# Optimization experiments

Hardware: AMD Instinct MI355X
Metric: run time of the kernel (lower is better)

The kernel has to match this reference:

```python
import jax, jax.numpy as jnp
import numpy as np

HEAD = 8  # number of attention heads (init kwarg)


def setup_inputs() -> dict:
    key = jax.random.key(0)
    k1, k2, k3 = jax.random.split(key, 3)
    b, H, W, c = 8, 32, 32, 512
    dim = 512
    x = jax.random.normal(k1, (b, H, W, c), dtype=jnp.float32)
    # 1x1 Conv == per-pixel matmul over channels
    w_qkv = jax.random.normal(k2, (c, 3 * dim), dtype=jnp.float32) * (c ** -0.5)
    w_out = jax.random.normal(k3, (dim, dim), dtype=jnp.float32) * (dim ** -0.5)
    b_out = jnp.zeros((dim,), dtype=jnp.float32)
    return {"x": x, "w_qkv": w_qkv, "w_out": w_out, "b_out": b_out}


def reference(x, w_qkv, w_out, b_out):
    b, H, W, c = x.shape
    n = H * W
    # QKV 1x1-conv projection (no bias)
    qkv = jnp.einsum('bhwc,cd->bhwd', x, w_qkv)          # (b, H, W, 3*dim)
    qkv = qkv.reshape(b, n, HEAD, -1)                     # (b, n, head, 3*dh)
    q, k, v = jnp.split(qkv, 3, axis=-1)                  # each (b, n, head, dh)
    scale = b ** -0.5  # NOTE: source scales by batch size, reproduced faithfully
    attn = jax.nn.softmax(jnp.einsum('bihd,bjhd->bhij', q, k) * scale, axis=-1)
    out = jnp.einsum('bhij,bjhd->bihd', attn, v)          # (b, n, head, dh)
    out = out.reshape(b, H, W, -1)                        # (b, H, W, dim)
    # output 1x1-conv projection (with bias)
    return jnp.einsum('bhwc,cd->bhwd', out, w_out) + b_out
```

## Files before the change

kernel.cpp:

```cpp
#include <hip/hip_runtime.h>
#include <hip/hip_bf16.h>

typedef __bf16 bf16x8_t __attribute__((ext_vector_type(8)));
typedef float  f32x4_t  __attribute__((ext_vector_type(4)));
typedef short  s16x8_t  __attribute__((ext_vector_type(8)));

#define NTOK   1024
#define CDIM   512
#define QKVDIM 1536
#define NHEAD  8
#define DHEAD  64
#define C1EXP  0.51007088f
#define C2EXP  34.624681f

__device__ __forceinline__ float b2f(short s) {
    unsigned int u = ((unsigned int)(unsigned short)s) << 16;
    float f; __builtin_memcpy(&f, &u, 4); return f;
}
__device__ __forceinline__ short f2b(float f) {
    __bf16 h = (__bf16)f; short s; __builtin_memcpy(&s, &h, 2); return s;
}

__global__ __launch_bounds__(256) void cvt_fused(
    const float* __restrict__ x, const float* __restrict__ wq,
    short* __restrict__ xb, short* __restrict__ wqbT)
{
    int bid = blockIdx.x;
    if (bid < 2048) {
        int i = bid * 256 + threadIdx.x;
        const float* p = x + (size_t)i * 8;
        float4 a = *(const float4*)p, b = *(const float4*)(p + 4);
        s16x8_t v;
        v[0]=f2b(a.x); v[1]=f2b(a.y); v[2]=f2b(a.z); v[3]=f2b(a.w);
        v[4]=f2b(b.x); v[5]=f2b(b.y); v[6]=f2b(b.z); v[7]=f2b(b.w);
        *(s16x8_t*)(xb + (size_t)i * 8) = v;
    } else {
        int i = (bid - 2048) * 256 + threadIdx.x;
        int k = i / QKVDIM, n = i % QKVDIM;
        wqbT[(size_t)n * 512 + k] = f2b(wq[i]);
    }
}

__global__ __launch_bounds__(256) void cvtT(const float* __restrict__ in,
                                            short* __restrict__ out,
                                            int K, int N)
{
    int i = blockIdx.x * 256 + threadIdx.x;
    if (i < K * N) {
        int k = i / N, n = i % N;
        out[(size_t)n * K + k] = f2b(in[i]);
    }
}

template <int N, bool BIAS, bool OUTF32>
__global__ __launch_bounds__(256) void gemm128(
    const short* __restrict__ A, const short* __restrict__ Bt,
    const float* __restrict__ bias, void* __restrict__ C)
{
    __shared__ __align__(16) short Al[128 * 64];
    __shared__ __align__(16) short Bl[128 * 64];

    const int t = threadIdx.x;
    const int N0 = blockIdx.x * 128, M0 = blockIdx.y * 128;
    const int w = t >> 6, lane = t & 63;
    const int quad = lane >> 4, mr = lane & 15;
    const int wm = (w >> 1) * 64, wn = (w & 1) * 64;

    int srow[4], soff[4];
#pragma unroll
    for (int r = 0; r < 4; ++r) {
        int ci = r * 256 + t;
        srow[r] = ci >> 3;
        soff[r] = (ci & 7) * 8;
    }
    const short* Ag = A  + (size_t)M0 * 512;
    const short* Bg = Bt + (size_t)N0 * 512;

    s16x8_t ar[4], br[4];
#pragma unroll
    for (int r = 0; r < 4; ++r) {
        ar[r] = *(const s16x8_t*)(Ag + (size_t)srow[r] * 512 + soff[r]);
        br[r] = *(const s16x8_t*)(Bg + (size_t)srow[r] * 512 + soff[r]);
    }

    f32x4_t acc[4][4];
#pragma unroll
    for (int ms = 0; ms < 4; ++ms)
#pragma unroll
        for (int ns = 0; ns < 4; ++ns) acc[ms][ns] = f32x4_t{0.f,0.f,0.f,0.f};

#pragma unroll 1
    for (int kc = 0; kc < 8; ++kc) {
        __syncthreads();
#pragma unroll
        for (int r = 0; r < 4; ++r) {
            int lds = srow[r] * 64 + (((soff[r] >> 3) ^ (srow[r] & 7)) * 8);
            *(s16x8_t*)(Al + lds) = ar[r];
            *(s16x8_t*)(Bl + lds) = br[r];
        }
        __syncthreads();
        if (kc < 7) {
            int k0 = (kc + 1) * 64;
#pragma unroll
            for (int r = 0; r < 4; ++r) {
                ar[r] = *(const s16x8_t*)(Ag + (size_t)srow[r] * 512 + k0 + soff[r]);
                br[r] = *(const s16x8_t*)(Bg + (size_t)srow[r] * 512 + k0 + soff[r]);
            }
        }
#pragma unroll
        for (int kh = 0; kh < 2; ++kh) {
            bf16x8_t af[4], bf[4];
#pragma unroll
            for (int ms = 0; ms < 4; ++ms) {
                int rr = wm + ms * 16 + mr;
                af[ms] = *(const bf16x8_t*)(Al + rr * 64 + (((kh * 4 + quad) ^ (rr & 7)) * 8));
            }
#pragma unroll
            for (int ns = 0; ns < 4; ++ns) {
                int rr = wn + ns * 16 + mr;
                bf[ns] = *(const bf16x8_t*)(Bl + rr * 64 + (((kh * 4 + quad) ^ (rr & 7)) * 8));
            }
#pragma unroll
            for (int ms = 0; ms < 4; ++ms)
#pragma unroll
                for (int ns = 0; ns < 4; ++ns)
                    acc[ms][ns] = __builtin_amdgcn_mfma_f32_16x16x32_bf16(
                        af[ms], bf[ns], acc[ms][ns], 0, 0, 0);
        }
    }

#pragma unroll
    for (int ms = 0; ms < 4; ++ms) {
        int row = M0 + wm + ms * 16 + quad * 4;
#pragma unroll
        for (int ns = 0; ns < 4; ++ns) {
            int col = N0 + wn + ns * 16 + mr;
            float bz = BIAS ? bias[col] : 0.f;
#pragma unroll
            for (int i = 0; i < 4; ++i) {
                if constexpr (OUTF32)
                    ((float*)C)[(size_t)(row + i) * N + col] = acc[ms][ns][i] + bz;
                else
                    ((short*)C)[(size_t)(row + i) * N + col] = f2b(acc[ms][ns][i]);
            }
        }
    }
}

__global__ __launch_bounds__(256) void attn_mfma(
    const short* __restrict__ qkv, short* __restrict__ aout)
{
    __shared__ __align__(16) short Kb[2][64 * 72];
    __shared__ __align__(16) short Vb[2][64 * 72];
    __shared__ __align__(16) short Pl[4][32 * 72];

    const int t = threadIdx.x;
    const int g = blockIdx.x;
    const int qb = (g >> 3) & 7;
    const int bh = ((g >> 6) << 3) | (g & 7);
    const int h = bh & 7, b = bh >> 3;
    const int w = t >> 6, lane = t & 63;
    const int quad = lane >> 4, mr = lane & 15;

    bf16x8_t qf[2][2];
#pragma unroll
    for (int ms = 0; ms < 2; ++ms) {
        size_t qrow = (size_t)(b * NTOK + qb * 128 + w * 32 + ms * 16 + mr) * QKVDIM + h * 192;
        qf[ms][0] = *(const bf16x8_t*)(qkv + qrow + quad * 8);
        qf[ms][1] = *(const bf16x8_t*)(qkv + qrow + 32 + quad * 8);
    }

    float lsum[2][4] = {};
    f32x4_t O[2][4];
#pragma unroll
    for (int ms = 0; ms < 2; ++ms)
#pragma unroll
        for (int d = 0; d < 4; ++d) O[ms][d] = f32x4_t{0.f, 0.f, 0.f, 0.f};

    short* Pw = Pl[w];

    const int j0i = t >> 3, j1i = j0i + 32, d8 = (t & 7) * 8;
    const int pjb0 = ((j0i >> 3) ^ (t & 7)) * 8 + (j0i & 7);
    const int pjb1 = ((j1i >> 3) ^ (t & 7)) * 8 + (j1i & 7);

    s16x8_t k0r, v0r, k1r, v1r;
    {
        size_t b0 = (size_t)(b * NTOK + j0i) * QKVDIM + h * 192;
        size_t b1 = (size_t)(b * NTOK + j1i) * QKVDIM + h * 192;
        k0r = *(const s16x8_t*)(qkv + b0 + 64 + d8);
        v0r = *(const s16x8_t*)(qkv + b0 + 128 + d8);
        k1r = *(const s16x8_t*)(qkv + b1 + 64 + d8);
        v1r = *(const s16x8_t*)(qkv + b1 + 128 + d8);
    }

#pragma unroll 1
    for (int jt = 0; jt < 16; ++jt) {
        const int cur = jt & 1;
        short* Kl = Kb[cur];
        short* Vt = Vb[cur];
        *(s16x8_t*)(Kl + j0i * 72 + d8) = k0r;
        *(s16x8_t*)(Kl + j1i * 72 + d8) = k1r;
#pragma unroll
        for (int i = 0; i < 8; ++i) {
            Vt[(d8 + i) * 72 + pjb0] = v0r[i];
            Vt[(d8 + i) * 72 + pjb1] = v1r[i];
        }
        __syncthreads();

        if (jt < 15) {
            size_t b0 = (size_t)(b * NTOK + (jt + 1) * 64 + j0i) * QKVDIM + h * 192;
            size_t b1 = (size_t)(b * NTOK + (jt + 1) * 64 + j1i) * QKVDIM + h * 192;
            k0r = *(const s16x8_t*)(qkv + b0 + 64 + d8);
            v0r = *(const s16x8_t*)(qkv + b0 + 128 + d8);
            k1r = *(const s16x8_t*)(qkv + b1 + 64 + d8);
            v1r = *(const s16x8_t*)(qkv + b1 + 128 + d8);
        }

#pragma unroll
        for (int ms = 0; ms < 2; ++ms) {
            f32x4_t s[4];
#pragma unroll
            for (int js = 0; js < 4; ++js) {
                const short* kb = Kl + (js * 16 + mr) * 72 + quad * 8;
                f32x4_t a0 = __builtin_amdgcn_mfma_f32_16x16x32_bf16(
                    qf[ms][0], *(const bf16x8_t*)kb, f32x4_t{0.f,0.f,0.f,0.f}, 0, 0, 0);
                s[js] = __builtin_amdgcn_mfma_f32_16x16x32_bf16(
                    qf[ms][1], *(const bf16x8_t*)(kb + 32), a0, 0, 0, 0);
            }

            short ph[4][4];
#pragma unroll
            for (int js = 0; js < 4; ++js)
#pragma unroll
                for (int r = 0; r < 4; ++r) {
                    short hh = f2b(__builtin_amdgcn_exp2f(s[js][r] * C1EXP - C2EXP));
                    ph[js][r] = hh;
                    lsum[ms][r] += b2f(hh);
                }

            short* Pm = Pw + ms * 16 * 72;
#pragma unroll
            for (int js = 0; js < 4; ++js)
#pragma unroll
                for (int r = 0; r < 4; ++r)
                    Pm[(quad * 4 + r) * 72 +
                       (((js * 2 + (mr >> 3)) + 2 * quad) & 7) * 8 + (mr & 7)] = ph[js][r];
            bf16x8_t pa0 = *(const bf16x8_t*)(Pm + mr * 72 + ((quad     + 2 * (mr >> 2)) & 7) * 8);
            bf16x8_t pa1 = *(const bf16x8_t*)(Pm + mr * 72 + ((quad + 4 + 2 * (mr >> 2)) & 7) * 8);

#pragma unroll
            for (int d = 0; d < 4; ++d) {
                int R = d * 16 + mr;
                int rx = (R >> 3) & 7;
                const short* vb0 = Vt + R * 72 + ((quad ^ rx) * 8);
                const short* vb1 = Vt + R * 72 + (((4 + quad) ^ rx) * 8);
                O[ms][d] = __builtin_amdgcn_mfma_f32_16x16x32_bf16(
                    pa0, *(const bf16x8_t*)vb0, O[ms][d], 0, 0, 0);
                O[ms][d] = __builtin_amdgcn_mfma_f32_16x16x32_bf16(
                    pa1, *(const bf16x8_t*)vb1, O[ms][d], 0, 0, 0);
            }
        }
    }

#pragma unroll
    for (int ms = 0; ms < 2; ++ms)
#pragma unroll
        for (int r = 0; r < 4; ++r) {
            float l = lsum[ms][r];
#pragma unroll
            for (int off = 1; off < 16; off <<= 1) l += __shfl_xor(l, off);
            float inv = 1.f / l;
            size_t tok = (size_t)(b * NTOK + qb * 128 + w * 32 + ms * 16 + quad * 4 + r);
#pragma unroll
            for (int d = 0; d < 4; ++d)
                aout[tok * CDIM + h * DHEAD + d * 16 + mr] = f2b(O[ms][d][r] * inv);
        }
}

extern "C" void kernel_launch(void* const* d_in, const int* in_sizes, int n_in,
                              void* d_out, int out_size, void* d_ws, size_t ws_size,
                              hipStream_t stream)
{
    const float* x     = (const float*)d_in[0];
    const float* w_qkv = (const float*)d_in[1];
    const float* w_out = (const float*)d_in[2];
    const float* b_out = (const float*)d_in[3];
    for (int i = 0; i < n_in; ++i) {
        if      (in_sizes[i] == 4194304) x     = (const float*)d_in[i];
        else if (in_sizes[i] ==  786432) w_qkv = (const float*)d_in[i];
        else if (in_sizes[i] ==  262144) w_out = (const float*)d_in[i];
        else if (in_sizes[i] ==     512) b_out = (const float*)d_in[i];
    }

    short* qkv  = (short*)d_ws;
    short* aout = (short*)((char*)d_ws + (size_t)8192 * QKVDIM * 2);
    short* xb   = (short*)d_out;
    short* wqbT = (short*)d_out + (size_t)8192 * 512;
    short* wobT = (short*)d_ws;

    cvt_fused<<<5120, 256, 0, stream>>>(x, w_qkv, xb, wqbT);

    gemm128<QKVDIM, false, false>
        <<<dim3(QKVDIM / 128, 8192 / 128), 256, 0, stream>>>(xb, wqbT, nullptr, qkv);

    attn_mfma<<<512, 256, 0, stream>>>(qkv, aout);

    cvtT<<<1024, 256, 0, stream>>>(w_out, wobT, 512, 512);

    gemm128<CDIM, true, true>
        <<<dim3(CDIM / 128, 8192 / 128), 256, 0, stream>>>(aout, wobT, b_out, d_out);
}
```

Baseline: 152.1 us.

## Emit transposed V from QKV GEMM and simplify attention to 64-query tiles

The QKV GEMM epilogue now splits its output into a packed Q/K buffer and a per-head transposed V buffer. This lets the attention kernel load V with plain vector stores to LDS instead of scalar transposing writes. The attention kernel is restructured to 16 query rows per wave and 64 queries per block, doubling the grid to 1024 blocks. It drops LDS double buffering in favour of a second barrier and computes S transposed so P can be written with vector stores. The trade-off is more K/V reloads from global memory and strided scattered writes for V in the GEMM epilogue.

```diff
diff --git a/kernel.cpp b/kernel.cpp
--- a/kernel.cpp
+++ b/kernel.cpp
@@ -3,6 +3,7 @@
 
 typedef __bf16 bf16x8_t __attribute__((ext_vector_type(8)));
 typedef float  f32x4_t  __attribute__((ext_vector_type(4)));
+typedef short  s16x4_t  __attribute__((ext_vector_type(4)));
 typedef short  s16x8_t  __attribute__((ext_vector_type(8)));
 
 #define NTOK   1024
@@ -52,11 +53,11 @@
     }
 }
 
-template <int N, bool BIAS, bool OUTF32>
-__global__ __launch_bounds__(256) void gemm128(
+__global__ __launch_bounds__(256) void gemm_qkv(
     const short* __restrict__ A, const short* __restrict__ Bt,
-    const float* __restrict__ bias, void* __restrict__ C)
-{
+    short* __restrict__ qk, short* __restrict__ vT)
+{
+    constexpr int N = QKVDIM;
     __shared__ __align__(16) short Al[128 * 64];
     __shared__ __align__(16) short Bl[128 * 64];
 
@@ -132,6 +133,106 @@
 #pragma unroll
     for (int ms = 0; ms < 4; ++ms) {
         int row = M0 + wm + ms * 16 + quad * 4;
+        int bb = row >> 10, ti = row & 1023;
+#pragma unroll
+        for (int ns = 0; ns < 4; ++ns) {
+            int c0 = N0 + wn + ns * 16;
+            int hh = c0 / 192, r0 = c0 % 192;
+            if (r0 < 128) {
+                size_t base = (size_t)row * 1024 + hh * 128 + r0 + mr;
+#pragma unroll
+                for (int i = 0; i < 4; ++i)
+                    qk[base + (size_t)i * 1024] = f2b(acc[ms][ns][i]);
+            } else {
+                s16x4_t v4;
+#pragma unroll
+                for (int i = 0; i < 4; ++i) v4[i] = f2b(acc[ms][ns][i]);
+                *(s16x4_t*)(vT + ((size_t)(bb * 8 + hh) * 64 + (r0 - 128) + mr) * 1024 + ti) = v4;
+            }
+        }
+    }
+}
+
+template <int N, bool BIAS, bool OUTF32>
+__global__ __launch_bounds__(256) void gemm128(
+    const short* __restrict__ A, const short* __restrict__ Bt,
+    const float* __restrict__ bias, void* __restrict__ C)
+{
+    __shared__ __align__(16) short Al[128 * 64];
+    __shared__ __align__(16) short Bl[128 * 64];
+
+    const int t = threadIdx.x;
+    const int N0 = blockIdx.x * 128, M0 = blockIdx.y * 128;
+    const int w = t >> 6, lane = t & 63;
+    const int quad = lane >> 4, mr = lane & 15;
+    const int wm = (w >> 1) * 64, wn = (w & 1) * 64;
+
+    int srow[4], soff[4];
+#pragma unroll
+    for (int r = 0; r < 4; ++r) {
+        int ci = r * 256 + t;
+        srow[r] = ci >> 3;
+        soff[r] = (ci & 7) * 8;
+    }
+    const short* Ag = A  + (size_t)M0 * 512;
+    const short* Bg = Bt + (size_t)N0 * 512;
+
+    s16x8_t ar[4], br[4];
+#pragma unroll
+    for (int r = 0; r < 4; ++r) {
+        ar[r] = *(const s16x8_t*)(Ag + (size_t)srow[r] * 512 + soff[r]);
+        br[r] = *(const s16x8_t*)(Bg + (size_t)srow[r] * 512 + soff[r]);
+    }
+
+    f32x4_t acc[4][4];
+#pragma unroll
+    for (int ms = 0; ms < 4; ++ms)
+#pragma unroll
+        for (int ns = 0; ns < 4; ++ns) acc[ms][ns] = f32x4_t{0.f,0.f,0.f,0.f};
+
+#pragma unroll 1
+    for (int kc = 0; kc < 8; ++kc) {
+        __syncthreads();
+#pragma unroll
+        for (int r = 0; r < 4; ++r) {
+            int lds = srow[r] * 64 + (((soff[r] >> 3) ^ (srow[r] & 7)) * 8);
+            *(s16x8_t*)(Al + lds) = ar[r];
+            *(s16x8_t*)(Bl + lds) = br[r];
+        }
+        __syncthreads();
+        if (kc < 7) {
+            int k0 = (kc + 1) * 64;
+#pragma unroll
+            for (int r = 0; r < 4; ++r) {
+                ar[r] = *(const s16x8_t*)(Ag + (size_t)srow[r] * 512 + k0 + soff[r]);
+                br[r] = *(const s16x8_t*)(Bg + (size_t)srow[r] * 512 + k0 + soff[r]);
+            }
+        }
+#pragma unroll
+        for (int kh = 0; kh < 2; ++kh) {
+            bf16x8_t af[4], bf[4];
+#pragma unroll
+            for (int ms = 0; ms < 4; ++ms) {
+                int rr = wm + ms * 16 + mr;
+                af[ms] = *(const bf16x8_t*)(Al + rr * 64 + (((kh * 4 + quad) ^ (rr & 7)) * 8));
+            }
+#pragma unroll
+            for (int ns = 0; ns < 4; ++ns) {
+                int rr = wn + ns * 16 + mr;
+                bf[ns] = *(const bf16x8_t*)(Bl + rr * 64 + (((kh * 4 + quad) ^ (rr & 7)) * 8));
+            }
+#pragma unroll
+            for (int ms = 0; ms < 4; ++ms)
+#pragma unroll
+                for (int ns = 0; ns < 4; ++ns)
+                    acc[ms][ns] = __builtin_amdgcn_mfma_f32_16x16x32_bf16(
+                        af[ms], bf[ns], acc[ms][ns], 0, 0, 0);
+        }
+    }
+
+#pragma unroll
+    for (int ms = 0; ms < 4; ++ms) {
+        int row = M0 + wm + ms * 16 + quad * 4;
 #pragma unroll
         for (int ns = 0; ns < 4; ++ns) {
             int col = N0 + wn + ns * 16 + mr;
@@ -147,134 +248,106 @@
     }
 }
 
-__global__ __launch_bounds__(256) void attn_mfma(
-    const short* __restrict__ qkv, short* __restrict__ aout)
-{
-    __shared__ __align__(16) short Kb[2][64 * 72];
-    __shared__ __align__(16) short Vb[2][64 * 72];
-    __shared__ __align__(16) short Pl[4][32 * 72];
+__global__ __launch_bounds__(256) void attn_st(
+    const short* __restrict__ qk, const short* __restrict__ vT,
+    short* __restrict__ aout)
+{
+    __shared__ __align__(16) short Kl[64 * 72];
+    __shared__ __align__(16) short Vt[64 * 72];
+    __shared__ __align__(16) short Pl[4][16 * 72];
 
     const int t = threadIdx.x;
     const int g = blockIdx.x;
-    const int qb = (g >> 3) & 7;
-    const int bh = ((g >> 6) << 3) | (g & 7);
+    const int qt = (g >> 3) & 15;
+    const int bh = ((g >> 7) << 3) | (g & 7);
     const int h = bh & 7, b = bh >> 3;
     const int w = t >> 6, lane = t & 63;
     const int quad = lane >> 4, mr = lane & 15;
 
-    bf16x8_t qf[2][2];
-#pragma unroll
-    for (int ms = 0; ms < 2; ++ms) {
-        size_t qrow = (size_t)(b * NTOK + qb * 128 + w * 32 + ms * 16 + mr) * QKVDIM + h * 192;
-        qf[ms][0] = *(const bf16x8_t*)(qkv + qrow + quad * 8);
-        qf[ms][1] = *(const bf16x8_t*)(qkv + qrow + 32 + quad * 8);
-    }
-
-    float lsum[2][4] = {};
-    f32x4_t O[2][4];
-#pragma unroll
-    for (int ms = 0; ms < 2; ++ms)
-#pragma unroll
-        for (int d = 0; d < 4; ++d) O[ms][d] = f32x4_t{0.f, 0.f, 0.f, 0.f};
-
-    short* Pw = Pl[w];
-
-    const int j0i = t >> 3, j1i = j0i + 32, d8 = (t & 7) * 8;
-    const int pjb0 = ((j0i >> 3) ^ (t & 7)) * 8 + (j0i & 7);
-    const int pjb1 = ((j1i >> 3) ^ (t & 7)) * 8 + (j1i & 7);
-
-    s16x8_t k0r, v0r, k1r, v1r;
-    {
-        size_t b0 = (size_t)(b * NTOK + j0i) * QKVDIM + h * 192;
-        size_t b1 = (size_t)(b * NTOK + j1i) * QKVDIM + h * 192;
-        k0r = *(const s16x8_t*)(qkv + b0 + 64 + d8);
-        v0r = *(const s16x8_t*)(qkv + b0 + 128 + d8);
-        k1r = *(const s16x8_t*)(qkv + b1 + 64 + d8);
-        v1r = *(const s16x8_t*)(qkv + b1 + 128 + d8);
-    }
+    const size_t qbase = (size_t)(b * NTOK + qt * 64 + w * 16 + mr) * 1024 + h * 128;
+    const bf16x8_t qf0 = *(const bf16x8_t*)(qk + qbase + quad * 8);
+    const bf16x8_t qf1 = *(const bf16x8_t*)(qk + qbase + 32 + quad * 8);
+
+    float lsum = 0.f;
+    f32x4_t O[4];
+#pragma unroll
+    for (int d = 0; d < 4; ++d) O[d] = f32x4_t{0.f, 0.f, 0.f, 0.f};
+
+    short* Pm = Pl[w];
+
+    const int r0i = t >> 3, r1i = r0i + 32, c8 = (t & 7) * 8;
+    const size_t kgbase = (size_t)(b * NTOK) * 1024 + h * 128 + 64 + c8;
+    const size_t vgbase = (size_t)(b * 8 + h) * 64 * 1024 + c8;
+
+    s16x8_t k0r, k1r, v0r, v1r;
+    k0r = *(const s16x8_t*)(qk + kgbase + (size_t)r0i * 1024);
+    k1r = *(const s16x8_t*)(qk + kgbase + (size_t)r1i * 1024);
+    v0r = *(const s16x8_t*)(vT + vgbase + (size_t)r0i * 1024);
+    v1r = *(const s16x8_t*)(vT + vgbase + (size_t)r1i * 1024);
 
 #pragma unroll 1
     for (int jt = 0; jt < 16; ++jt) {
-        const int cur = jt & 1;
-        short* Kl = Kb[cur];
-        short* Vt = Vb[cur];
-        *(s16x8_t*)(Kl + j0i * 72 + d8) = k0r;
-        *(s16x8_t*)(Kl + j1i * 72 + d8) = k1r;
-#pragma unroll
-        for (int i = 0; i < 8; ++i) {
-            Vt[(d8 + i) * 72 + pjb0] = v0r[i];
-            Vt[(d8 + i) * 72 + pjb1] = v1r[i];
-        }
+        *(s16x8_t*)(Kl + r0i * 72 + c8) = k0r;
+        *(s16x8_t*)(Kl + r1i * 72 + c8) = k1r;
+        *(s16x8_t*)(Vt + r0i * 72 + c8) = v0r;
+        *(s16x8_t*)(Vt + r1i * 72 + c8) = v1r;
         __syncthreads();
 
         if (jt < 15) {
-            size_t b0 = (size_t)(b * NTOK + (jt + 1) * 64 + j0i) * QKVDIM + h * 192;
-            size_t b1 = (size_t)(b * NTOK + (jt + 1) * 64 + j1i) * QKVDIM + h * 192;
-            k0r = *(const s16x8_t*)(qkv + b0 + 64 + d8);
-            v0r = *(const s16x8_t*)(qkv + b0 + 128 + d8);
-            k1r = *(const s16x8_t*)(qkv + b1 + 64 + d8);
-            v1r = *(const s16x8_t*)(qkv + b1 + 128 + d8);
-        }
-
-#pragma unroll
-        for (int ms = 0; ms < 2; ++ms) {
-            f32x4_t s[4];
-#pragma unroll
-            for (int js = 0; js < 4; ++js) {
-                const short* kb = Kl + (js * 16 + mr) * 72 + quad * 8;
-                f32x4_t a0 = __builtin_amdgcn_mfma_f32_16x16x32_bf16(
-                    qf[ms][0], *(const bf16x8_t*)kb, f32x4_t{0.f,0.f,0.f,0.f}, 0, 0, 0);
-                s[js] = __builtin_amdgcn_mfma_f32_16x16x32_bf16(
-                    qf[ms][1], *(const bf16x8_t*)(kb + 32), a0, 0, 0, 0);
-            }
-
-            short ph[4][4];
-#pragma unroll
-            for (int js = 0; js < 4; ++js)
-#pragma unroll
-                for (int r = 0; r < 4; ++r) {
-                    short hh = f2b(__builtin_amdgcn_exp2f(s[js][r] * C1EXP - C2EXP));
-                    ph[js][r] = hh;
-                    lsum[ms][r] += b2f(hh);
-                }
-
-            short* Pm = Pw + ms * 16 * 72;
-#pragma unroll
-            for (int js = 0; js < 4; ++js)
-#pragma unroll
-                for (int r = 0; r < 4; ++r)
-                    Pm[(quad * 4 + r) * 72 +
-                       (((js * 2 + (mr >> 3)) + 2 * quad) & 7) * 8 + (mr & 7)] = ph[js][r];
-            bf16x8_t pa0 = *(const bf16x8_t*)(Pm + mr * 72 + ((quad     + 2 * (mr >> 2)) & 7) * 8);
-            bf16x8_t pa1 = *(const bf16x8_t*)(Pm + mr * 72 + ((quad + 4 + 2 * (mr >> 2)) & 7) * 8);
-
-#pragma unroll
-            for (int d = 0; d < 4; ++d) {
-                int R = d * 16 + mr;
-                int rx = (R >> 3) & 7;
-                const short* vb0 = Vt + R * 72 + ((quad ^ rx) * 8);
-                const short* vb1 = Vt + R * 72 + (((4 + quad) ^ rx) * 8);
-                O[ms][d] = __builtin_amdgcn_mfma_f32_16x16x32_bf16(
-                    pa0, *(const bf16x8_t*)vb0, O[ms][d], 0, 0, 0);
-                O[ms][d] = __builtin_amdgcn_mfma_f32_16x16x32_bf16(
-                    pa1, *(const bf16x8_t*)vb1, O[ms][d], 0, 0, 0);
-            }
-        }
-    }
-
-#pragma unroll
-    for (int ms = 0; ms < 2; ++ms)
-#pragma unroll
-        for (int r = 0; r < 4; ++r) {
-            float l = lsum[ms][r];
-#pragma unroll
-            for (int off = 1; off < 16; off <<= 1) l += __shfl_xor(l, off);
-            float inv = 1.f / l;
-            size_t tok = (size_t)(b * NTOK + qb * 128 + w * 32 + ms * 16 + quad * 4 + r);
-#pragma unroll
-            for (int d = 0; d < 4; ++d)
-                aout[tok * CDIM + h * DHEAD + d * 16 + mr] = f2b(O[ms][d][r] * inv);
-        }
+            int j0n = (jt + 1) * 64;
+            k0r = *(const s16x8_t*)(qk + kgbase + (size_t)(j0n + r0i) * 1024);
+            k1r = *(const s16x8_t*)(qk + kgbase + (size_t)(j0n + r1i) * 1024);
+            v0r = *(const s16x8_t*)(vT + vgbase + (size_t)r0i * 1024 + j0n);
+            v1r = *(const s16x8_t*)(vT + vgbase + (size_t)r1i * 1024 + j0n);
+        }
+
+        f32x4_t s[4];
+#pragma unroll
+        for (int jj = 0; jj < 4; ++jj) {
+            const short* kb = Kl + (jj * 16 + mr) * 72 + quad * 8;
+            f32x4_t a0 = __builtin_amdgcn_mfma_f32_16x16x32_bf16(
+                *(const bf16x8_t*)kb, qf0, f32x4_t{0.f,0.f,0.f,0.f}, 0, 0, 0);
+            s[jj] = __builtin_amdgcn_mfma_f32_16x16x32_bf16(
+                *(const bf16x8_t*)(kb + 32), qf1, a0, 0, 0, 0);
+        }
+
+#pragma unroll
+        for (int jj = 0; jj < 4; ++jj) {
+            s16x4_t pv;
+#pragma unroll
+            for (int r = 0; r < 4; ++r) {
+                short hh = f2b(__builtin_amdgcn_exp2f(s[jj][r] * C1EXP - C2EXP));
+                pv[r] = hh;
+                lsum += b2f(hh);
+            }
+            *(s16x4_t*)(Pm + mr * 72 + jj * 16 + quad * 4) = pv;
+        }
+
+        bf16x8_t pa0 = *(const bf16x8_t*)(Pm + mr * 72 + quad * 8);
+        bf16x8_t pa1 = *(const bf16x8_t*)(Pm + mr * 72 + 32 + quad * 8);
+
+#pragma unroll
+        for (int dt = 0; dt < 4; ++dt) {
+            const short* vb = Vt + (dt * 16 + mr) * 72 + quad * 8;
+            O[dt] = __builtin_amdgcn_mfma_f32_16x16x32_bf16(
+                pa0, *(const bf16x8_t*)vb, O[dt], 0, 0, 0);
+            O[dt] = __builtin_amdgcn_mfma_f32_16x16x32_bf16(
+                pa1, *(const bf16x8_t*)(vb + 32), O[dt], 0, 0, 0);
+        }
+        __syncthreads();
+    }
+
+    lsum += __shfl_xor(lsum, 16, 64);
+    lsum += __shfl_xor(lsum, 32, 64);
+#pragma unroll
+    for (int i = 0; i < 4; ++i) {
+        float li = __shfl(lsum, quad * 4 + i, 64);
+        float inv = 1.f / li;
+        size_t tok = (size_t)(b * NTOK + qt * 64 + w * 16 + quad * 4 + i);
+#pragma unroll
+        for (int dt = 0; dt < 4; ++dt)
+            aout[tok * CDIM + h * DHEAD + dt * 16 + mr] = f2b(O[dt][i] * inv);
+    }
 }
 
 extern "C" void kernel_launch(void* const* d_in, const int* in_sizes, int n_in,
@@ -292,18 +365,18 @@
         else if (in_sizes[i] ==     512) b_out = (const float*)d_in[i];
     }
 
-    short* qkv  = (short*)d_ws;
-    short* aout = (short*)((char*)d_ws + (size_t)8192 * QKVDIM * 2);
+    short* qk   = (short*)d_ws;
+    short* vT   = (short*)((char*)d_ws + (size_t)8192 * 1024 * 2);
+    short* aout = (short*)((char*)d_ws + (size_t)8192 * 1024 * 2 + (size_t)64 * 64 * 1024 * 2);
     short* xb   = (short*)d_out;
     short* wqbT = (short*)d_out + (size_t)8192 * 512;
     short* wobT = (short*)d_ws;
 
     cvt_fused<<<5120, 256, 0, stream>>>(x, w_qkv, xb, wqbT);
 
-    gemm128<QKVDIM, false, false>
-        <<<dim3(QKVDIM / 128, 8192 / 128), 256, 0, stream>>>(xb, wqbT, nullptr, qkv);
-
-    attn_mfma<<<512, 256, 0, stream>>>(qkv, aout);
+    gemm_qkv<<<dim3(QKVDIM / 128, 8192 / 128), 256, 0, stream>>>(xb, wqbT, qk, vT);
+
+    attn_st<<<1024, 256, 0, stream>>>(qk, vT, aout);
 
     cvtT<<<1024, 256, 0, stream>>>(w_out, wobT, 512, 512);
 
```

Measured after the change: 148.7 us. -2.3%, faster.
